# Kernel tuning notes

Measured on AMD Instinct MI355X. Metric: run time of the kernel, lower is better.

The kernel has to match this reference:

```python
import jax, jax.numpy as jnp
import numpy as np


def pan_conv(x, edge_index, filter_w, lin_w, lin_b):
    """Faithful dense equivalent of PANConv.

    panentropy: pan = w0*I + w1*A + w2*A^2 (filter_size terms).
    PyG then extracts nonzero edges (row=source j, col=target i), computes
    deg = count of pan-edges per row, norm = deg^-1/2[row]*deg^-1/2[col],
    and scatter-adds norm*edge_weight*x_j at target i. Dense form:
      out = d[:,None] * (pan.T @ (d[:,None] * (x @ W.T + b)))
    where d[i] = (row-nnz of pan)^-0.5.
    """
    n = x.shape[0]
    dt = x.dtype
    adj = jnp.zeros((n, n), dt).at[edge_index[0], edge_index[1]].set(1.0)
    eye = jnp.eye(n, dtype=dt)
    pan = filter_w[0] * eye
    tmp = eye
    for i in range(1, filter_w.shape[0]):  # small fixed filter_size loop
        tmp = tmp @ adj
        pan = pan + filter_w[i] * tmp
    # degree() in the original counts edge occurrences = nnz per row of pan
    deg = jnp.sum(pan != 0, axis=1).astype(dt)
    dinv = jnp.where(deg > 0, jax.lax.rsqrt(jnp.maximum(deg, 1.0)), 0.0)
    h = x @ lin_w.T + lin_b  # [n, out_channels]
    return dinv[:, None] * (pan.T @ (dinv[:, None] * h))


def setup_inputs() -> dict:
    key = jax.random.key(0)
    ks = jax.random.split(key, 4)
    N, E, F_IN, H, C = 2048, 32768, 512, 16, 32
    x = jax.random.normal(ks[0], (N, F_IN), jnp.float32)
    edge_index = jax.random.randint(ks[1], (2, E), 0, N, jnp.int32)
    fw1 = 0.1 * jnp.ones(3, jnp.float32)
    fw2 = 0.1 * jnp.ones(3, jnp.float32)
    lin1_w = jax.random.normal(ks[2], (H, F_IN), jnp.float32) / np.sqrt(F_IN).astype(np.float32)
    lin1_b = jnp.zeros(H, jnp.float32)
    lin2_w = jax.random.normal(ks[3], (C, H), jnp.float32) / np.sqrt(H).astype(np.float32)
    lin2_b = jnp.zeros(C, jnp.float32)
    return dict(x=x, edge_index=edge_index, fw1=fw1, lin1_w=lin1_w, lin1_b=lin1_b,
                fw2=fw2, lin2_w=lin2_w, lin2_b=lin2_b)


def reference(x, edge_index, fw1, lin1_w, lin1_b, fw2, lin2_w, lin2_b):
    h = pan_conv(x, edge_index, fw1, lin1_w, lin1_b)
    h = jax.nn.relu(h)  # dropout is identity in eval mode
    h = pan_conv(h, edge_index, fw2, lin2_w, lin2_b)
    return jax.nn.log_softmax(h, axis=1)
```

## Files before the change

kernel.cpp:

```cpp
#include <hip/hip_runtime.h>
#include <hip/hip_bf16.h>

#define NN 2048
#define NW 64

__global__ void k_zero_r9(unsigned* __restrict__ p, int n) {
    int i = blockIdx.x * blockDim.x + threadIdx.x;
    int stride = gridDim.x * blockDim.x;
    for (; i < n; i += stride) p[i] = 0u;
}

__global__ void k_build_r9(const int* __restrict__ ei, int E,
                           unsigned* __restrict__ Abits, unsigned* __restrict__ ATbits) {
    int e = blockIdx.x * blockDim.x + threadIdx.x;
    if (e >= E) return;
    int s = ei[e] & (NN - 1);
    int d = ei[E + e] & (NN - 1);
    atomicOr(&Abits[s * NW + (d >> 5)], 1u << (d & 31));
    atomicOr(&ATbits[d * NW + (s >> 5)], 1u << (s & 31));
}

__global__ void __launch_bounds__(256) k_pandeg_r9(
        const unsigned* __restrict__ Abits,
        const float* __restrict__ fw1, const float* __restrict__ fw2,
        float* __restrict__ dinv1, float* __restrict__ dinv2) {
    __shared__ int cnt[NN];
    __shared__ unsigned rowbits[NW];
    __shared__ int neigh[NN];
    __shared__ int ncnt;
    __shared__ int red1[4], red2[4];

    int i = blockIdx.x, tid = threadIdx.x;
    for (int j = tid; j < NN; j += 256) cnt[j] = 0;
    if (tid < NW) rowbits[tid] = Abits[i * NW + tid];
    if (tid == 0) ncnt = 0;
    __syncthreads();

    if (tid < NW) {
        unsigned bits = rowbits[tid];
        while (bits) {
            int b = __ffs(bits) - 1; bits &= bits - 1;
            int slot = atomicAdd(&ncnt, 1);
            if (slot < NN) neigh[slot] = tid * 32 + b;
        }
    }
    __syncthreads();

    int lane = tid & 63, grp = tid >> 6;
    int nc = ncnt < NN ? ncnt : NN;
    for (int n = grp; n < nc; n += 4) {
        int k = neigh[n];
        unsigned bits = Abits[k * NW + lane];
        while (bits) {
            int b = __ffs(bits) - 1; bits &= bits - 1;
            atomicAdd(&cnt[lane * 32 + b], 1);
        }
    }
    __syncthreads();

    float w10 = fw1[0], w11 = fw1[1], w12 = fw1[2];
    float w20 = fw2[0], w21 = fw2[1], w22 = fw2[2];
    int c1 = 0, c2 = 0;
    for (int j = tid; j < NN; j += 256) {
        float a = ((rowbits[j >> 5] >> (j & 31)) & 1u) ? 1.f : 0.f;
        float c = (float)cnt[j];
        float dg = (j == i) ? 1.f : 0.f;
        c1 += ((w10 * dg + w11 * a + w12 * c) != 0.f);
        c2 += ((w20 * dg + w21 * a + w22 * c) != 0.f);
    }
    for (int o = 32; o; o >>= 1) { c1 += __shfl_down(c1, o); c2 += __shfl_down(c2, o); }
    if (lane == 0) { red1[grp] = c1; red2[grp] = c2; }
    __syncthreads();
    if (tid == 0) {
        int d1 = red1[0] + red1[1] + red1[2] + red1[3];
        int d2 = red2[0] + red2[1] + red2[2] + red2[3];
        dinv1[i] = d1 > 0 ? rsqrtf((float)d1) : 0.f;
        dinv2[i] = d2 > 0 ? rsqrtf((float)d2) : 0.f;
    }
}

__global__ void __launch_bounds__(256) k_lin1_r9(
        const float* __restrict__ x, const float* __restrict__ W,
        const float* __restrict__ b, const float* __restrict__ dinv,
        float* __restrict__ y) {
    __shared__ float xs[528];
    int i = blockIdx.x, tid = threadIdx.x;
    if (tid < 128) {
        float4 v = ((const float4*)(x + i * 512))[tid];
        int f = tid * 4;
        int m = f + (f >> 5);
        xs[m] = v.x; xs[m + 1] = v.y; xs[m + 2] = v.z; xs[m + 3] = v.w;
    }
    __syncthreads();
    int c = tid >> 4, seg = tid & 15;
    const float* wr = W + c * 512 + seg * 32;
    const float* xr = xs + seg * 33;
    float s = 0.f;
#pragma unroll
    for (int f = 0; f < 32; f++) s += xr[f] * wr[f];
    for (int o = 8; o; o >>= 1) s += __shfl_down(s, o, 16);
    if (seg == 0) y[i * 16 + c] = dinv[i] * (s + b[c]);
}

__global__ void __launch_bounds__(256) k_spmm16_r9(
        const unsigned* __restrict__ ATbits, const float* __restrict__ y,
        float* __restrict__ t) {
    __shared__ int neigh[4][64];
    __shared__ int ncnt[4];
    int tid = threadIdx.x, w = tid >> 6, lane = tid & 63;
    int i = blockIdx.x * 4 + w;
    if (lane == 0) ncnt[w] = 0;
    __syncthreads();
    unsigned bits = ATbits[i * NW + lane];
    while (bits) {
        int b = __ffs(bits) - 1; bits &= bits - 1;
        int slot = atomicAdd(&ncnt[w], 1);
        if (slot < 64) neigh[w][slot] = lane * 32 + b;
    }
    __syncthreads();
    int nc = ncnt[w] < 64 ? ncnt[w] : 64;
    int c = lane & 15, grp = lane >> 4;
    float acc = 0.f;
    for (int n = grp; n < nc; n += 4) acc += y[neigh[w][n] * 16 + c];
    acc += __shfl_down(acc, 32);
    acc += __shfl_down(acc, 16);
    if (lane < 16) t[i * 16 + c] = acc;
}

__global__ void __launch_bounds__(256) k_final1_lin2_r9(
        const unsigned* __restrict__ ATbits, const float* __restrict__ y,
        const float* __restrict__ t, const float* __restrict__ dinv1,
        const float* __restrict__ dinv2, const float* __restrict__ fw,
        const float* __restrict__ W2, const float* __restrict__ b2,
        float* __restrict__ y2) {
    __shared__ int neigh[4][64];
    __shared__ int ncnt[4];
    int tid = threadIdx.x, w = tid >> 6, lane = tid & 63;
    int i = blockIdx.x * 4 + w;
    if (lane == 0) ncnt[w] = 0;
    __syncthreads();
    unsigned bits = ATbits[i * NW + lane];
    while (bits) {
        int b = __ffs(bits) - 1; bits &= bits - 1;
        int slot = atomicAdd(&ncnt[w], 1);
        if (slot < 64) neigh[w][slot] = lane * 32 + b;
    }
    __syncthreads();
    int nc = ncnt[w] < 64 ? ncnt[w] : 64;
    int c = lane & 15, grp = lane >> 4;
    float acc = 0.f;
    for (int n = grp; n < nc; n += 4) acc += t[neigh[w][n] * 16 + c];
    acc += __shfl_down(acc, 32);
    acc += __shfl_down(acc, 16);
    float z = fw[0] * y[i * 16 + c] + fw[1] * t[i * 16 + c] + fw[2] * acc;
    z *= dinv1[i];
    z = z > 0.f ? z : 0.f;
    float s2 = 0.f;
#pragma unroll
    for (int f = 0; f < 16; f++) s2 += __shfl(z, f) * W2[lane * 16 + f];
    if (lane < 32) y2[i * 32 + lane] = dinv2[i] * (s2 + b2[lane]);
}

__global__ void __launch_bounds__(256) k_spmm32_r9(
        const unsigned* __restrict__ ATbits, const float* __restrict__ y,
        float* __restrict__ t) {
    __shared__ int neigh[4][64];
    __shared__ int ncnt[4];
    int tid = threadIdx.x, w = tid >> 6, lane = tid & 63;
    int i = blockIdx.x * 4 + w;
    if (lane == 0) ncnt[w] = 0;
    __syncthreads();
    unsigned bits = ATbits[i * NW + lane];
    while (bits) {
        int b = __ffs(bits) - 1; bits &= bits - 1;
        int slot = atomicAdd(&ncnt[w], 1);
        if (slot < 64) neigh[w][slot] = lane * 32 + b;
    }
    __syncthreads();
    int nc = ncnt[w] < 64 ? ncnt[w] : 64;
    int c = lane & 31, grp = lane >> 5;
    float acc = 0.f;
    for (int n = grp; n < nc; n += 2) acc += y[neigh[w][n] * 32 + c];
    acc += __shfl_down(acc, 32);
    if (lane < 32) t[i * 32 + c] = acc;
}

__global__ void __launch_bounds__(256) k_final2_r9(
        const unsigned* __restrict__ ATbits, const float* __restrict__ y,
        const float* __restrict__ t, const float* __restrict__ dinv,
        const float* __restrict__ fw, float* __restrict__ out) {
    __shared__ int neigh[4][64];
    __shared__ int ncnt[4];
    int tid = threadIdx.x, w = tid >> 6, lane = tid & 63;
    int i = blockIdx.x * 4 + w;
    if (lane == 0) ncnt[w] = 0;
    __syncthreads();
    unsigned bits = ATbits[i * NW + lane];
    while (bits) {
        int b = __ffs(bits) - 1; bits &= bits - 1;
        int slot = atomicAdd(&ncnt[w], 1);
        if (slot < 64) neigh[w][slot] = lane * 32 + b;
    }
    __syncthreads();
    int nc = ncnt[w] < 64 ? ncnt[w] : 64;
    int c = lane & 31, grp = lane >> 5;
    float acc = 0.f;
    for (int n = grp; n < nc; n += 2) acc += t[neigh[w][n] * 32 + c];
    acc += __shfl_down(acc, 32);
    float o = dinv[i] * (fw[0] * y[i * 32 + c] + fw[1] * t[i * 32 + c] + fw[2] * acc);
    float m = o;
    for (int k = 16; k; k >>= 1) m = fmaxf(m, __shfl_xor(m, k, 32));
    float e = expf(o - m);
    float ssum = e;
    for (int k = 16; k; k >>= 1) ssum += __shfl_xor(ssum, k, 32);
    if (lane < 32) out[i * 32 + c] = o - m - logf(ssum);
}

extern "C" void kernel_launch(void* const* d_in, const int* in_sizes, int n_in,
                              void* d_out, int out_size, void* d_ws, size_t ws_size,
                              hipStream_t stream) {
    const float* x   = (const float*)d_in[0];
    const int*   ei  = (const int*)d_in[1];
    const float* fw1 = (const float*)d_in[2];
    const float* W1  = (const float*)d_in[3];
    const float* b1  = (const float*)d_in[4];
    const float* fw2 = (const float*)d_in[5];
    const float* W2  = (const float*)d_in[6];
    const float* b2  = (const float*)d_in[7];
    float* out = (float*)d_out;
    int E = in_sizes[1] / 2;

    char* ws = (char*)d_ws;
    size_t off = 0;
    auto alloc = [&](size_t bytes) { void* p = ws + off; off += (bytes + 255) & ~size_t(255); return p; };
    unsigned* Abits  = (unsigned*)alloc(NN * NW * 4);
    unsigned* ATbits = (unsigned*)alloc(NN * NW * 4);
    float* dinv1 = (float*)alloc(NN * 4);
    float* dinv2 = (float*)alloc(NN * 4);
    float* y1 = (float*)alloc(NN * 16 * 4);
    float* t1 = (float*)alloc(NN * 16 * 4);
    float* y2 = (float*)alloc(NN * 32 * 4);
    float* t2 = (float*)alloc(NN * 32 * 4);
    (void)ws_size; (void)n_in; (void)out_size;

    k_zero_r9<<<256, 256, 0, stream>>>(Abits, 2 * NN * NW);
    k_build_r9<<<(E + 255) / 256, 256, 0, stream>>>(ei, E, Abits, ATbits);
    k_pandeg_r9<<<NN, 256, 0, stream>>>(Abits, fw1, fw2, dinv1, dinv2);

    k_lin1_r9<<<NN, 256, 0, stream>>>(x, W1, b1, dinv1, y1);
    k_spmm16_r9<<<NN / 4, 256, 0, stream>>>(ATbits, y1, t1);
    k_final1_lin2_r9<<<NN / 4, 256, 0, stream>>>(ATbits, y1, t1, dinv1, dinv2,
                                                 fw1, W2, b2, y2);
    k_spmm32_r9<<<NN / 4, 256, 0, stream>>>(ATbits, y2, t2);
    k_final2_r9<<<NN / 4, 256, 0, stream>>>(ATbits, y2, t2, dinv2, fw2, out);
}
```

Measured before the change: 111.9 us.

## Compute A^2 row counts with wave-level bit-sliced counters instead of shared atomics

The pan-degree kernel now gives each row one 64-lane wave instead of a whole 256-thread block. It accumulates per-column A^2 path counts as a 7-bit bit-sliced counter held in registers, updated by ripple-carry XOR/AND on bitset words, which replaces the shared-memory histogram, neighbour list and atomicAdds. Nonzero pan entries are then found with bitmask logic, including an exact-cancellation check when w1 + w2*c can equal zero, and counted with popc. This removes the shared-memory atomics and block syncs and launches a quarter as many blocks, but counts above 127 would wrap.

```diff
diff --git a/kernel.cpp b/kernel.cpp
--- a/kernel.cpp
+++ b/kernel.cpp
@@ -4,14 +4,14 @@
 #define NN 2048
 #define NW 64
 
-__global__ void k_zero_r9(unsigned* __restrict__ p, int n) {
+__global__ void k_zero_r10(unsigned* __restrict__ p, int n) {
     int i = blockIdx.x * blockDim.x + threadIdx.x;
     int stride = gridDim.x * blockDim.x;
     for (; i < n; i += stride) p[i] = 0u;
 }
 
-__global__ void k_build_r9(const int* __restrict__ ei, int E,
-                           unsigned* __restrict__ Abits, unsigned* __restrict__ ATbits) {
+__global__ void k_build_r10(const int* __restrict__ ei, int E,
+                            unsigned* __restrict__ Abits, unsigned* __restrict__ ATbits) {
     int e = blockIdx.x * blockDim.x + threadIdx.x;
     if (e >= E) return;
     int s = ei[e] & (NN - 1);
@@ -20,66 +20,76 @@
     atomicOr(&ATbits[d * NW + (s >> 5)], 1u << (s & 31));
 }
 
-__global__ void __launch_bounds__(256) k_pandeg_r9(
+__global__ void __launch_bounds__(256) k_pandeg_r10(
         const unsigned* __restrict__ Abits,
         const float* __restrict__ fw1, const float* __restrict__ fw2,
         float* __restrict__ dinv1, float* __restrict__ dinv2) {
-    __shared__ int cnt[NN];
-    __shared__ unsigned rowbits[NW];
-    __shared__ int neigh[NN];
-    __shared__ int ncnt;
-    __shared__ int red1[4], red2[4];
-
-    int i = blockIdx.x, tid = threadIdx.x;
-    for (int j = tid; j < NN; j += 256) cnt[j] = 0;
-    if (tid < NW) rowbits[tid] = Abits[i * NW + tid];
-    if (tid == 0) ncnt = 0;
-    __syncthreads();
-
-    if (tid < NW) {
-        unsigned bits = rowbits[tid];
-        while (bits) {
-            int b = __ffs(bits) - 1; bits &= bits - 1;
-            int slot = atomicAdd(&ncnt, 1);
-            if (slot < NN) neigh[slot] = tid * 32 + b;
+    int tid = threadIdx.x, lane = tid & 63;
+    int i = blockIdx.x * 4 + (tid >> 6);
+    unsigned row = Abits[i * NW + lane];
+    unsigned b0 = 0, b1 = 0, b2 = 0, b3 = 0, b4 = 0, b5 = 0, b6 = 0;
+    for (int wi = 0; wi < NW; wi++) {
+        unsigned wv = __shfl(row, wi);
+        while (wv) {
+            int bb = __ffs(wv) - 1; wv &= wv - 1;
+            unsigned carry = Abits[(wi * 32 + bb) * NW + lane], t;
+            t = b0 ^ carry; carry &= b0; b0 = t;
+            t = b1 ^ carry; carry &= b1; b1 = t;
+            t = b2 ^ carry; carry &= b2; b2 = t;
+            t = b3 ^ carry; carry &= b3; b3 = t;
+            t = b4 ^ carry; carry &= b4; b4 = t;
+            t = b5 ^ carry; carry &= b5; b5 = t;
+            b6 ^= carry;
         }
     }
-    __syncthreads();
-
-    int lane = tid & 63, grp = tid >> 6;
-    int nc = ncnt < NN ? ncnt : NN;
-    for (int n = grp; n < nc; n += 4) {
-        int k = neigh[n];
-        unsigned bits = Abits[k * NW + lane];
-        while (bits) {
-            int b = __ffs(bits) - 1; bits &= bits - 1;
-            atomicAdd(&cnt[lane * 32 + b], 1);
-        }
-    }
-    __syncthreads();
-
-    float w10 = fw1[0], w11 = fw1[1], w12 = fw1[2];
-    float w20 = fw2[0], w21 = fw2[1], w22 = fw2[2];
-    int c1 = 0, c2 = 0;
-    for (int j = tid; j < NN; j += 256) {
-        float a = ((rowbits[j >> 5] >> (j & 31)) & 1u) ? 1.f : 0.f;
-        float c = (float)cnt[j];
-        float dg = (j == i) ? 1.f : 0.f;
-        c1 += ((w10 * dg + w11 * a + w12 * c) != 0.f);
-        c2 += ((w20 * dg + w21 * a + w22 * c) != 0.f);
-    }
+    unsigned nz = b0 | b1 | b2 | b3 | b4 | b5 | b6;
+    int dl = i >> 5, db = i & 31;
+    unsigned ci = ((b0 >> db) & 1u) | (((b1 >> db) & 1u) << 1) | (((b2 >> db) & 1u) << 2)
+                | (((b3 >> db) & 1u) << 3) | (((b4 >> db) & 1u) << 4)
+                | (((b5 >> db) & 1u) << 5) | (((b6 >> db) & 1u) << 6);
+
+    float ws[6] = { fw1[0], fw1[1], fw1[2], fw2[0], fw2[1], fw2[2] };
+    int cnts[2];
+#pragma unroll
+    for (int setk = 0; setk < 2; setk++) {
+        float w0 = ws[setk * 3], w1 = ws[setk * 3 + 1], w2 = ws[setk * 3 + 2];
+        unsigned m;
+        bool useA = (w1 != 0.f), useC = (w2 != 0.f);
+        if (useA && useC) {
+            m = row | nz;
+            float c0f = -w1 / w2;
+            int c0 = (int)rintf(c0f);
+            if (c0 >= 1 && c0 <= 127 && fabsf(c0f - (float)c0) < 1e-5f) {
+                unsigned eq = 0xFFFFFFFFu;
+                eq &= (c0 & 1)  ? b0 : ~b0;
+                eq &= (c0 & 2)  ? b1 : ~b1;
+                eq &= (c0 & 4)  ? b2 : ~b2;
+                eq &= (c0 & 8)  ? b3 : ~b3;
+                eq &= (c0 & 16) ? b4 : ~b4;
+                eq &= (c0 & 32) ? b5 : ~b5;
+                eq &= (c0 & 64) ? b6 : ~b6;
+                m &= ~(row & eq);
+            }
+        } else if (useA) m = row;
+        else if (useC)   m = nz;
+        else             m = 0u;
+        int cnt;
+        if (lane == dl) {
+            unsigned a = (row >> db) & 1u;
+            float pv = w0 + w1 * (float)a + w2 * (float)ci;
+            cnt = __popc(m & ~(1u << db)) + (pv != 0.f ? 1 : 0);
+        } else cnt = __popc(m);
+        cnts[setk] = cnt;
+    }
+    int c1 = cnts[0], c2 = cnts[1];
     for (int o = 32; o; o >>= 1) { c1 += __shfl_down(c1, o); c2 += __shfl_down(c2, o); }
-    if (lane == 0) { red1[grp] = c1; red2[grp] = c2; }
-    __syncthreads();
-    if (tid == 0) {
-        int d1 = red1[0] + red1[1] + red1[2] + red1[3];
-        int d2 = red2[0] + red2[1] + red2[2] + red2[3];
-        dinv1[i] = d1 > 0 ? rsqrtf((float)d1) : 0.f;
-        dinv2[i] = d2 > 0 ? rsqrtf((float)d2) : 0.f;
-    }
-}
-
-__global__ void __launch_bounds__(256) k_lin1_r9(
+    if (lane == 0) {
+        dinv1[i] = c1 > 0 ? rsqrtf((float)c1) : 0.f;
+        dinv2[i] = c2 > 0 ? rsqrtf((float)c2) : 0.f;
+    }
+}
+
+__global__ void __launch_bounds__(256) k_lin1_r10(
         const float* __restrict__ x, const float* __restrict__ W,
         const float* __restrict__ b, const float* __restrict__ dinv,
         float* __restrict__ y) {
@@ -102,7 +112,7 @@
     if (seg == 0) y[i * 16 + c] = dinv[i] * (s + b[c]);
 }
 
-__global__ void __launch_bounds__(256) k_spmm16_r9(
+__global__ void __launch_bounds__(256) k_spmm16_r10(
         const unsigned* __restrict__ ATbits, const float* __restrict__ y,
         float* __restrict__ t) {
     __shared__ int neigh[4][64];
@@ -127,7 +137,7 @@
     if (lane < 16) t[i * 16 + c] = acc;
 }
 
-__global__ void __launch_bounds__(256) k_final1_lin2_r9(
+__global__ void __launch_bounds__(256) k_final1_lin2_r10(
         const unsigned* __restrict__ ATbits, const float* __restrict__ y,
         const float* __restrict__ t, const float* __restrict__ dinv1,
         const float* __restrict__ dinv2, const float* __restrict__ fw,
@@ -161,7 +171,7 @@
     if (lane < 32) y2[i * 32 + lane] = dinv2[i] * (s2 + b2[lane]);
 }
 
-__global__ void __launch_bounds__(256) k_spmm32_r9(
+__global__ void __launch_bounds__(256) k_spmm32_r10(
         const unsigned* __restrict__ ATbits, const float* __restrict__ y,
         float* __restrict__ t) {
     __shared__ int neigh[4][64];
@@ -185,7 +195,7 @@
     if (lane < 32) t[i * 32 + c] = acc;
 }
 
-__global__ void __launch_bounds__(256) k_final2_r9(
+__global__ void __launch_bounds__(256) k_final2_r10(
         const unsigned* __restrict__ ATbits, const float* __restrict__ y,
         const float* __restrict__ t, const float* __restrict__ dinv,
         const float* __restrict__ fw, float* __restrict__ out) {
@@ -243,14 +253,14 @@
     float* t2 = (float*)alloc(NN * 32 * 4);
     (void)ws_size; (void)n_in; (void)out_size;
 
-    k_zero_r9<<<256, 256, 0, stream>>>(Abits, 2 * NN * NW);
-    k_build_r9<<<(E + 255) / 256, 256, 0, stream>>>(ei, E, Abits, ATbits);
-    k_pandeg_r9<<<NN, 256, 0, stream>>>(Abits, fw1, fw2, dinv1, dinv2);
-
-    k_lin1_r9<<<NN, 256, 0, stream>>>(x, W1, b1, dinv1, y1);
-    k_spmm16_r9<<<NN / 4, 256, 0, stream>>>(ATbits, y1, t1);
-    k_final1_lin2_r9<<<NN / 4, 256, 0, stream>>>(ATbits, y1, t1, dinv1, dinv2,
-                                                 fw1, W2, b2, y2);
-    k_spmm32_r9<<<NN / 4, 256, 0, stream>>>(ATbits, y2, t2);
-    k_final2_r9<<<NN / 4, 256, 0, stream>>>(ATbits, y2, t2, dinv2, fw2, out);
-}
+    k_zero_r10<<<256, 256, 0, stream>>>(Abits, 2 * NN * NW);
+    k_build_r10<<<(E + 255) / 256, 256, 0, stream>>>(ei, E, Abits, ATbits);
+    k_pandeg_r10<<<NN / 4, 256, 0, stream>>>(Abits, fw1, fw2, dinv1, dinv2);
+
+    k_lin1_r10<<<NN, 256, 0, stream>>>(x, W1, b1, dinv1, y1);
+    k_spmm16_r10<<<NN / 4, 256, 0, stream>>>(ATbits, y1, t1);
+    k_final1_lin2_r10<<<NN / 4, 256, 0, stream>>>(ATbits, y1, t1, dinv1, dinv2,
+                                                  fw1, W2, b2, y2);
+    k_spmm32_r10<<<NN / 4, 256, 0, stream>>>(ATbits, y2, t2);
+    k_final2_r10<<<NN / 4, 256, 0, stream>>>(ATbits, y2, t2, dinv2, fw2, out);
+}
```

Measured after the change: 114.3 us. 2.1% more time.
